# Kernel tuning notes

Measured on AMD Instinct MI355X. Metric: run time of the kernel, lower is better.

The kernel has to match this reference:

```python
import jax, jax.numpy as jnp
import numpy as np


def setup_inputs() -> dict:
    key = jax.random.key(0)
    ks = jax.random.split(key, 6)
    B, L, C = 32, 336, 512
    t = L // 2 + 1  # 169 rfft frequencies; four_l must equal t
    s = 1.0 / np.sqrt(C)
    return {
        "x": jax.random.normal(ks[0], (B, L, C), jnp.float32),
        "Wr": jax.random.normal(ks[1], (t, C, C), jnp.float32) * s,  # real part of complex Linear weights [t, out, in]
        "Wi": jax.random.normal(ks[2], (t, C, C), jnp.float32) * s,  # imag part
        "br": jax.random.normal(ks[3], (t, C), jnp.float32) * s,
        "bi": jax.random.normal(ks[4], (t, C), jnp.float32) * s,
        "weights": jax.random.normal(ks[5], (t,), jnp.float32),
    }


def reference(x, Wr, Wi, br, bi, weights):
    # x: [B, L, C] real. rfft along time with ortho norm -> [B, t, C] complex.
    B, L, C = x.shape
    t = Wr.shape[0]
    n = 2 * (t - 1)  # torch irfft default output length (== L, L even)
    xf = jnp.fft.rfft(x, axis=1, norm='ortho')  # [B, t, C] complex64

    # Per-frequency complex linear: y[b,i,o] = sum_c xf[b,i,c] * W[i,o,c] + b[i,o].
    # This fuses the original repeat + eye-mask + python loop into one batched GEMM.
    W = Wr + 1j * Wi
    b = br + 1j * bi
    y = jnp.einsum('bic,ioc->bio', xf, W) + b[None]  # [B, t, C]

    # The original builds fre[b,i,:,c] as a spectrum that is one-hot at frequency i
    # (value y[b,i,c]) and irffts along the frequency axis (ortho norm). For a one-hot
    # spectrum: irfft(onehot_i * y)[l] = scale_i * Re(y * exp(2*pi*j*i*l/n)) / sqrt(n),
    # with scale_i = 2 except at DC (i=0) and Nyquist (i=t-1) where it is 1
    # (imag parts of DC/Nyquist bins are discarded by C2R, matching torch).
    # Finally ConcatenationWithLearnableCoefficient sums over i with softmax weights,
    # so we fold softmax(weights) * scale_i / sqrt(n) into one coefficient per i.
    i_idx = jnp.arange(t)
    scale = jnp.where((i_idx == 0) | (i_idx == t - 1), 1.0, 2.0).astype(jnp.float32)
    w = jax.nn.softmax(weights)
    coef = w * scale / jnp.sqrt(jnp.float32(n))  # [t]

    l_idx = jnp.arange(n)
    theta = (2.0 * jnp.pi / n) * (i_idx[:, None] * l_idx[None, :]).astype(jnp.float32)  # [t, n]
    cos_m, sin_m = jnp.cos(theta), jnp.sin(theta)

    yr = y.real * coef[None, :, None]
    yi = y.imag * coef[None, :, None]
    # Re(y * e^{j theta}) = yr*cos - yi*sin ; sum over frequencies i -> [B, n, C]
    out = jnp.einsum('bic,il->blc', yr, cos_m) - jnp.einsum('bic,il->blc', yi, sin_m)
    return out
```

## Files before the change

kernel.cpp:

```cpp
#include <hip/hip_runtime.h>
#include <math.h>

typedef short   s16x8  __attribute__((ext_vector_type(8)));
typedef __bf16  bf16x8 __attribute__((ext_vector_type(8)));
typedef float   f32x4  __attribute__((ext_vector_type(4)));

#define T_FREQ 169
#define NN     336
#define CCH    512
#define BB     32
#define TP     176
#define LP     352
#define KP     192

static constexpr size_t OFF_COEF = 0;
static constexpr size_t OFF_FC   = 1024;
static constexpr size_t OFF_FS   = OFF_FC + 124928;
static constexpr size_t OFF_CCOS = OFF_FS + 124928;
static constexpr size_t OFF_CSIN = OFF_CCOS + 130048;
static constexpr size_t OFF_XT   = OFF_CSIN + 130048;
static constexpr size_t OFF_XR   = OFF_XT + (size_t)BB*CCH*LP*2;
static constexpr size_t OFF_XI   = OFF_XR + (size_t)TP*BB*CCH*2;
static constexpr size_t OFF_Y    = OFF_XI + (size_t)TP*BB*CCH*2;

__device__ __forceinline__ unsigned short f2bf(float f){
  unsigned u = __builtin_bit_cast(unsigned, f);
  u = (u + 0x7fffu + ((u >> 16) & 1u)) >> 16;
  return (unsigned short)u;
}

__device__ __forceinline__ f32x4 mfma16(bf16x8 a, bf16x8 b, f32x4 c){
  return __builtin_amdgcn_mfma_f32_16x16x32_bf16(a, b, c, 0, 0, 0);
}

__global__ __launch_bounds__(256) void prep_tables(const float* __restrict__ wts, char* ws){
  float* coef = (float*)(ws + OFF_COEF);
  unsigned short* Fc  = (unsigned short*)(ws + OFF_FC);
  unsigned short* Fs  = (unsigned short*)(ws + OFF_FS);
  unsigned short* Cc  = (unsigned short*)(ws + OFF_CCOS);
  unsigned short* Cs  = (unsigned short*)(ws + OFF_CSIN);
  const float PI2_N = 6.283185307179586f / (float)NN;
  const float inv_sqrt_n = 0.05455447255899809f;

  if (blockIdx.x == 0){
    __shared__ float red[256];
    int tid = threadIdx.x;
    float v = (tid < T_FREQ) ? wts[tid] : -1e30f;
    red[tid] = v; __syncthreads();
    for (int s = 128; s > 0; s >>= 1){ if (tid < s) red[tid] = fmaxf(red[tid], red[tid+s]); __syncthreads(); }
    float mx = red[0]; __syncthreads();
    float e = (tid < T_FREQ) ? expf(v - mx) : 0.f;
    red[tid] = e; __syncthreads();
    for (int s = 128; s > 0; s >>= 1){ if (tid < s) red[tid] += red[tid+s]; __syncthreads(); }
    float ssum = red[0];
    if (tid < T_FREQ){
      float sc = (tid == 0 || tid == T_FREQ-1) ? 1.f : 2.f;
      coef[tid] = (e / ssum) * sc * inv_sqrt_n;
    }
    return;
  }
  int gid = (blockIdx.x - 1) * 256 + threadIdx.x;
  int stride = (gridDim.x - 1) * 256;
  for (int e = gid; e < TP*LP; e += stride){
    int i = e / LP, l = e % LP;
    float c = 0.f, s = 0.f;
    if (l < NN){
      int m = (i * l) % NN;
      float sv, cv; sincosf(PI2_N * (float)m, &sv, &cv);
      c = cv * inv_sqrt_n; s = -sv * inv_sqrt_n;
    }
    Fc[e] = f2bf(c); Fs[e] = f2bf(s);
  }
  for (int e = gid; e < NN*KP; e += stride){
    int l = e / KP, i = e % KP;
    float c = 0.f, s = 0.f;
    if (i < T_FREQ){
      int m = (i * l) % NN;
      float sv, cv; sincosf(PI2_N * (float)m, &sv, &cv);
      c = cv; s = -sv;
    }
    Cc[e] = f2bf(c); Cs[e] = f2bf(s);
  }
}

__global__ __launch_bounds__(256) void transpose_x(const float* __restrict__ x, char* ws){
  unsigned short* xt = (unsigned short*)(ws + OFF_XT);
  __shared__ float tile[32][33];
  int bid = blockIdx.x;
  int b  = bid / (11*16);
  int rm = bid % (11*16);
  int lt = rm / 16, ct = rm % 16;
  int tx = threadIdx.x & 31, ty = threadIdx.x >> 5;
  #pragma unroll
  for (int k = 0; k < 4; ++k){
    int l = lt*32 + ty + k*8;
    int c = ct*32 + tx;
    float v = (l < NN) ? x[((size_t)b*NN + l)*CCH + c] : 0.f;
    tile[ty + k*8][tx] = v;
  }
  __syncthreads();
  #pragma unroll
  for (int k = 0; k < 4; ++k){
    int crow = ct*32 + ty + k*8;
    int lcol = lt*32 + tx;
    xt[((size_t)b*CCH + crow)*LP + lcol] = f2bf(tile[tx][ty + k*8]);
  }
}

__global__ __launch_bounds__(256) void stage_rfft(char* ws){
  const unsigned short* xt = (const unsigned short*)(ws + OFF_XT);
  const unsigned short* Fc = (const unsigned short*)(ws + OFF_FC);
  const unsigned short* Fs = (const unsigned short*)(ws + OFF_FS);
  unsigned short* xr = (unsigned short*)(ws + OFF_XR);
  unsigned short* xi = (unsigned short*)(ws + OFF_XI);

  int b  = blockIdx.x >> 3;
  int c0 = (blockIdx.x & 7) * 64;
  int tid = threadIdx.x, lane = tid & 63, wv = tid >> 6;
  int kg = lane >> 4, ln = lane & 15;
  int c = c0 + wv*16 + ln;

  f32x4 aR[11], aI[11];
  #pragma unroll
  for (int m = 0; m < 11; ++m){ aR[m] = (f32x4){0,0,0,0}; aI[m] = (f32x4){0,0,0,0}; }

  const unsigned short* xrow = xt + ((size_t)b*CCH + c)*LP;
  for (int kk = 0; kk < 11; ++kk){
    int ko = kk*32 + kg*8;
    bf16x8 bx = *(const bf16x8*)(xrow + ko);
    #pragma unroll
    for (int m = 0; m < 11; ++m){
      bf16x8 fc = *(const bf16x8*)(Fc + (size_t)(m*16 + ln)*LP + ko);
      bf16x8 fs = *(const bf16x8*)(Fs + (size_t)(m*16 + ln)*LP + ko);
      aR[m] = mfma16(fc, bx, aR[m]);
      aI[m] = mfma16(fs, bx, aI[m]);
    }
  }
  int rbase = kg*4;
  #pragma unroll
  for (int m = 0; m < 11; ++m){
    #pragma unroll
    for (int r = 0; r < 4; ++r){
      int i = m*16 + rbase + r;
      size_t off = ((size_t)i*BB + b)*CCH + c;
      xr[off] = f2bf(aR[m][r]);
      xi[off] = f2bf(aI[m][r]);
    }
  }
}

__global__ __launch_bounds__(256) void stage_cgemm(const float* __restrict__ Wr, const float* __restrict__ Wi,
                                                   const float* __restrict__ br, const float* __restrict__ bi,
                                                   char* ws){
  const unsigned short* xr = (const unsigned short*)(ws + OFF_XR);
  const unsigned short* xi = (const unsigned short*)(ws + OFF_XI);
  const float* coef = (const float*)(ws + OFF_COEF);
  unsigned int* y = (unsigned int*)(ws + OFF_Y);

  int i  = blockIdx.x >> 2;
  int nb = blockIdx.x & 3;
  int tid = threadIdx.x, lane = tid & 63, wv = tid >> 6;
  int kg = lane >> 4, ln = lane & 15;
  int o0 = nb*128 + wv*32;

  f32x4 accR[2][2], accI[2][2];
  #pragma unroll
  for (int m = 0; m < 2; ++m)
    #pragma unroll
    for (int n = 0; n < 2; ++n){ accR[m][n] = (f32x4){0,0,0,0}; accI[m][n] = (f32x4){0,0,0,0}; }

  const size_t wbase = (size_t)i * CCH * CCH;
  const size_t xbase = (size_t)i * BB * CCH;

  for (int kk = 0; kk < 16; ++kk){
    int ko = kk*32 + kg*8;
    bf16x8 ar[2], ai[2];
    #pragma unroll
    for (int mb = 0; mb < 2; ++mb){
      ar[mb] = *(const bf16x8*)(xr + xbase + (size_t)(mb*16 + ln)*CCH + ko);
      ai[mb] = *(const bf16x8*)(xi + xbase + (size_t)(mb*16 + ln)*CCH + ko);
    }
    #pragma unroll
    for (int nt = 0; nt < 2; ++nt){
      const float* wrp = Wr + wbase + (size_t)(o0 + nt*16 + ln)*CCH + ko;
      const float* wip = Wi + wbase + (size_t)(o0 + nt*16 + ln)*CCH + ko;
      float4 r0 = *(const float4*)(wrp);
      float4 r1 = *(const float4*)(wrp + 4);
      float4 i0 = *(const float4*)(wip);
      float4 i1 = *(const float4*)(wip + 4);
      s16x8 tr, ti;
      tr[0]=f2bf(r0.x); tr[1]=f2bf(r0.y); tr[2]=f2bf(r0.z); tr[3]=f2bf(r0.w);
      tr[4]=f2bf(r1.x); tr[5]=f2bf(r1.y); tr[6]=f2bf(r1.z); tr[7]=f2bf(r1.w);
      ti[0]=f2bf(i0.x); ti[1]=f2bf(i0.y); ti[2]=f2bf(i0.z); ti[3]=f2bf(i0.w);
      ti[4]=f2bf(i1.x); ti[5]=f2bf(i1.y); ti[6]=f2bf(i1.z); ti[7]=f2bf(i1.w);
      s16x8 tin = ti ^ (short)0x8000;
      bf16x8 bwr  = __builtin_bit_cast(bf16x8, tr);
      bf16x8 bwi  = __builtin_bit_cast(bf16x8, ti);
      bf16x8 bwin = __builtin_bit_cast(bf16x8, tin);
      #pragma unroll
      for (int mb = 0; mb < 2; ++mb){
        accR[mb][nt] = mfma16(ar[mb], bwr,  accR[mb][nt]);
        accR[mb][nt] = mfma16(ai[mb], bwin, accR[mb][nt]);
        accI[mb][nt] = mfma16(ar[mb], bwi,  accI[mb][nt]);
        accI[mb][nt] = mfma16(ai[mb], bwr,  accI[mb][nt]);
      }
    }
  }

  float cf = coef[i];
  #pragma unroll
  for (int nt = 0; nt < 2; ++nt){
    int o = o0 + nt*16 + ln;
    float fbr = br[(size_t)i*CCH + o];
    float fbi = bi[(size_t)i*CCH + o];
    #pragma unroll
    for (int mb = 0; mb < 2; ++mb){
      #pragma unroll
      for (int r = 0; r < 4; ++r){
        float vr = (accR[mb][nt][r] + fbr) * cf;
        float vi = (accI[mb][nt][r] + fbi) * cf;
        int bb = mb*16 + kg*4 + r;
        y[((size_t)bb*KP + i)*CCH + o] = (unsigned)f2bf(vr) | ((unsigned)f2bf(vi) << 16);
      }
    }
  }
}

__global__ __launch_bounds__(256) void stage_irfft(const char* ws_c, float* __restrict__ out){
  const char* ws = ws_c;
  const unsigned short* Cc = (const unsigned short*)(ws + OFF_CCOS);
  const unsigned short* Cs = (const unsigned short*)(ws + OFF_CSIN);
  const unsigned int* y = (const unsigned int*)(ws + OFF_Y);

  __shared__ unsigned short lr[64][40];
  __shared__ unsigned short li[64][40];

  int b  = blockIdx.x >> 3;
  int c0 = (blockIdx.x & 7) * 64;
  int tid = threadIdx.x, lane = tid & 63, wv = tid >> 6;
  int kg = lane >> 4, ln = lane & 15;

  f32x4 acc[21];
  #pragma unroll
  for (int m = 0; m < 21; ++m) acc[m] = (f32x4){0,0,0,0};

  for (int kk = 0; kk < 6; ++kk){
    if (kk) __syncthreads();
    #pragma unroll
    for (int q = 0; q < 8; ++q){
      int idx = q*256 + tid;
      int ir = idx >> 6, cc = idx & 63;
      int i = kk*32 + ir;
      unsigned u = (i < T_FREQ) ? y[((size_t)b*KP + i)*CCH + c0 + cc] : 0u;
      lr[cc][ir] = (unsigned short)(u & 0xffffu);
      li[cc][ir] = (unsigned short)(u >> 16);
    }
    __syncthreads();
    int ko = kk*32 + kg*8;
    bf16x8 blr = *(const bf16x8*)(&lr[wv*16 + ln][kg*8]);
    bf16x8 bli = *(const bf16x8*)(&li[wv*16 + ln][kg*8]);
    #pragma unroll
    for (int m = 0; m < 21; ++m){
      bf16x8 ac = *(const bf16x8*)(Cc + (size_t)(m*16 + ln)*KP + ko);
      bf16x8 as = *(const bf16x8*)(Cs + (size_t)(m*16 + ln)*KP + ko);
      acc[m] = mfma16(ac, blr, acc[m]);
      acc[m] = mfma16(as, bli, acc[m]);
    }
  }

  int cdst = c0 + wv*16 + ln;
  #pragma unroll
  for (int m = 0; m < 21; ++m){
    #pragma unroll
    for (int r = 0; r < 4; ++r){
      int l = m*16 + kg*4 + r;
      out[((size_t)b*NN + l)*CCH + cdst] = acc[m][r];
    }
  }
}

extern "C" void kernel_launch(void* const* d_in, const int* in_sizes, int n_in,
                              void* d_out, int out_size, void* d_ws, size_t ws_size,
                              hipStream_t stream){
  const float* x   = (const float*)d_in[0];
  const float* Wr  = (const float*)d_in[1];
  const float* Wi  = (const float*)d_in[2];
  const float* br  = (const float*)d_in[3];
  const float* bi  = (const float*)d_in[4];
  const float* wts = (const float*)d_in[5];
  char* ws = (char*)d_ws;

  prep_tables<<<257, 256, 0, stream>>>(wts, ws);
  transpose_x<<<32*11*16, 256, 0, stream>>>(x, ws);
  stage_rfft<<<256, 256, 0, stream>>>(ws);
  stage_cgemm<<<T_FREQ*4, 256, 0, stream>>>(Wr, Wi, br, bi, ws);
  stage_irfft<<<256, 256, 0, stream>>>(ws, (float*)d_out);
}
```

Baseline: 185.6 us.

## Split FFT stages across more blocks and pipeline weight loads in complex GEMM

The rfft and irfft stages now split their output-row tiles across twice as many blocks, with one overlapping tile computed redundantly, to raise occupancy and cut per-thread accumulator registers. The complex GEMM narrows each wave to 16 output columns, launches twice as many blocks, and double-buffers the fp32 weight loads one k-step ahead so memory latency overlaps MFMA work. Float-to-bf16 conversion now uses the compiler's native cast instead of manual bit rounding. The cost is some duplicated table reads and redundant tile work, plus less reuse of the x operand per block in the GEMM.

```diff
diff --git a/kernel.cpp b/kernel.cpp
--- a/kernel.cpp
+++ b/kernel.cpp
@@ -24,9 +24,14 @@
 static constexpr size_t OFF_Y    = OFF_XI + (size_t)TP*BB*CCH*2;
 
 __device__ __forceinline__ unsigned short f2bf(float f){
-  unsigned u = __builtin_bit_cast(unsigned, f);
-  u = (u + 0x7fffu + ((u >> 16) & 1u)) >> 16;
-  return (unsigned short)u;
+  return __builtin_bit_cast(unsigned short, (__bf16)f);
+}
+
+__device__ __forceinline__ bf16x8 cvt8(float4 lo, float4 hi){
+  bf16x8 r;
+  r[0]=(__bf16)lo.x; r[1]=(__bf16)lo.y; r[2]=(__bf16)lo.z; r[3]=(__bf16)lo.w;
+  r[4]=(__bf16)hi.x; r[5]=(__bf16)hi.y; r[6]=(__bf16)hi.z; r[7]=(__bf16)hi.w;
+  return r;
 }
 
 __device__ __forceinline__ f32x4 mfma16(bf16x8 a, bf16x8 b, f32x4 c){
@@ -114,40 +119,64 @@
   unsigned short* xr = (unsigned short*)(ws + OFF_XR);
   unsigned short* xi = (unsigned short*)(ws + OFF_XI);
 
-  int b  = blockIdx.x >> 3;
-  int c0 = (blockIdx.x & 7) * 64;
+  int bid = blockIdx.x;
+  int b  = bid >> 4;
+  int rm = bid & 15;
+  int c0 = (rm & 7) * 64;
+  int mh = rm >> 3;
+  int mbase = mh * 5;
   int tid = threadIdx.x, lane = tid & 63, wv = tid >> 6;
   int kg = lane >> 4, ln = lane & 15;
   int c = c0 + wv*16 + ln;
 
-  f32x4 aR[11], aI[11];
-  #pragma unroll
-  for (int m = 0; m < 11; ++m){ aR[m] = (f32x4){0,0,0,0}; aI[m] = (f32x4){0,0,0,0}; }
+  f32x4 aR[6], aI[6];
+  #pragma unroll
+  for (int m = 0; m < 6; ++m){ aR[m] = (f32x4){0,0,0,0}; aI[m] = (f32x4){0,0,0,0}; }
 
   const unsigned short* xrow = xt + ((size_t)b*CCH + c)*LP;
   for (int kk = 0; kk < 11; ++kk){
     int ko = kk*32 + kg*8;
     bf16x8 bx = *(const bf16x8*)(xrow + ko);
     #pragma unroll
-    for (int m = 0; m < 11; ++m){
-      bf16x8 fc = *(const bf16x8*)(Fc + (size_t)(m*16 + ln)*LP + ko);
-      bf16x8 fs = *(const bf16x8*)(Fs + (size_t)(m*16 + ln)*LP + ko);
+    for (int m = 0; m < 6; ++m){
+      bf16x8 fc = *(const bf16x8*)(Fc + (size_t)((mbase+m)*16 + ln)*LP + ko);
+      bf16x8 fs = *(const bf16x8*)(Fs + (size_t)((mbase+m)*16 + ln)*LP + ko);
       aR[m] = mfma16(fc, bx, aR[m]);
       aI[m] = mfma16(fs, bx, aI[m]);
     }
   }
   int rbase = kg*4;
   #pragma unroll
-  for (int m = 0; m < 11; ++m){
+  for (int m = 0; m < 6; ++m){
     #pragma unroll
     for (int r = 0; r < 4; ++r){
-      int i = m*16 + rbase + r;
+      int i = (mbase+m)*16 + rbase + r;
       size_t off = ((size_t)i*BB + b)*CCH + c;
       xr[off] = f2bf(aR[m][r]);
       xi[off] = f2bf(aI[m][r]);
     }
   }
 }
+
+#define CGEMM_COMPUTE(W0,W1,V0,V1,KK) do {                                   \
+    int ko_ = (KK)*32 + kb;                                                  \
+    bf16x8 ar0 = *(const bf16x8*)(xrb + (size_t)(ln)*CCH + ko_);             \
+    bf16x8 ar1 = *(const bf16x8*)(xrb + (size_t)(16+ln)*CCH + ko_);          \
+    bf16x8 ai0 = *(const bf16x8*)(xib + (size_t)(ln)*CCH + ko_);             \
+    bf16x8 ai1 = *(const bf16x8*)(xib + (size_t)(16+ln)*CCH + ko_);          \
+    bf16x8 bwr = cvt8(W0,W1);                                                \
+    bf16x8 bwi = cvt8(V0,V1);                                                \
+    bf16x8 bwin = __builtin_bit_cast(bf16x8,                                 \
+        (s16x8)(__builtin_bit_cast(s16x8,bwi) ^ (short)0x8000));             \
+    accR0 = mfma16(ar0, bwr,  accR0);                                        \
+    accR0 = mfma16(ai0, bwin, accR0);                                        \
+    accI0 = mfma16(ar0, bwi,  accI0);                                        \
+    accI0 = mfma16(ai0, bwr,  accI0);                                        \
+    accR1 = mfma16(ar1, bwr,  accR1);                                        \
+    accR1 = mfma16(ai1, bwin, accR1);                                        \
+    accI1 = mfma16(ar1, bwi,  accI1);                                        \
+    accI1 = mfma16(ai1, bwr,  accI1);                                        \
+  } while (0)
 
 __global__ __launch_bounds__(256) void stage_cgemm(const float* __restrict__ Wr, const float* __restrict__ Wi,
                                                    const float* __restrict__ br, const float* __restrict__ bi,
@@ -157,72 +186,56 @@
   const float* coef = (const float*)(ws + OFF_COEF);
   unsigned int* y = (unsigned int*)(ws + OFF_Y);
 
-  int i  = blockIdx.x >> 2;
-  int nb = blockIdx.x & 3;
+  int i  = blockIdx.x >> 3;
+  int nb = blockIdx.x & 7;
   int tid = threadIdx.x, lane = tid & 63, wv = tid >> 6;
   int kg = lane >> 4, ln = lane & 15;
-  int o0 = nb*128 + wv*32;
-
-  f32x4 accR[2][2], accI[2][2];
-  #pragma unroll
-  for (int m = 0; m < 2; ++m)
-    #pragma unroll
-    for (int n = 0; n < 2; ++n){ accR[m][n] = (f32x4){0,0,0,0}; accI[m][n] = (f32x4){0,0,0,0}; }
-
-  const size_t wbase = (size_t)i * CCH * CCH;
-  const size_t xbase = (size_t)i * BB * CCH;
-
-  for (int kk = 0; kk < 16; ++kk){
-    int ko = kk*32 + kg*8;
-    bf16x8 ar[2], ai[2];
-    #pragma unroll
-    for (int mb = 0; mb < 2; ++mb){
-      ar[mb] = *(const bf16x8*)(xr + xbase + (size_t)(mb*16 + ln)*CCH + ko);
-      ai[mb] = *(const bf16x8*)(xi + xbase + (size_t)(mb*16 + ln)*CCH + ko);
-    }
-    #pragma unroll
-    for (int nt = 0; nt < 2; ++nt){
-      const float* wrp = Wr + wbase + (size_t)(o0 + nt*16 + ln)*CCH + ko;
-      const float* wip = Wi + wbase + (size_t)(o0 + nt*16 + ln)*CCH + ko;
-      float4 r0 = *(const float4*)(wrp);
-      float4 r1 = *(const float4*)(wrp + 4);
-      float4 i0 = *(const float4*)(wip);
-      float4 i1 = *(const float4*)(wip + 4);
-      s16x8 tr, ti;
-      tr[0]=f2bf(r0.x); tr[1]=f2bf(r0.y); tr[2]=f2bf(r0.z); tr[3]=f2bf(r0.w);
-      tr[4]=f2bf(r1.x); tr[5]=f2bf(r1.y); tr[6]=f2bf(r1.z); tr[7]=f2bf(r1.w);
-      ti[0]=f2bf(i0.x); ti[1]=f2bf(i0.y); ti[2]=f2bf(i0.z); ti[3]=f2bf(i0.w);
-      ti[4]=f2bf(i1.x); ti[5]=f2bf(i1.y); ti[6]=f2bf(i1.z); ti[7]=f2bf(i1.w);
-      s16x8 tin = ti ^ (short)0x8000;
-      bf16x8 bwr  = __builtin_bit_cast(bf16x8, tr);
-      bf16x8 bwi  = __builtin_bit_cast(bf16x8, ti);
-      bf16x8 bwin = __builtin_bit_cast(bf16x8, tin);
-      #pragma unroll
-      for (int mb = 0; mb < 2; ++mb){
-        accR[mb][nt] = mfma16(ar[mb], bwr,  accR[mb][nt]);
-        accR[mb][nt] = mfma16(ai[mb], bwin, accR[mb][nt]);
-        accI[mb][nt] = mfma16(ar[mb], bwi,  accI[mb][nt]);
-        accI[mb][nt] = mfma16(ai[mb], bwr,  accI[mb][nt]);
-      }
-    }
-  }
-
-  float cf = coef[i];
-  #pragma unroll
-  for (int nt = 0; nt < 2; ++nt){
-    int o = o0 + nt*16 + ln;
-    float fbr = br[(size_t)i*CCH + o];
-    float fbi = bi[(size_t)i*CCH + o];
-    #pragma unroll
-    for (int mb = 0; mb < 2; ++mb){
-      #pragma unroll
-      for (int r = 0; r < 4; ++r){
-        float vr = (accR[mb][nt][r] + fbr) * cf;
-        float vi = (accI[mb][nt][r] + fbi) * cf;
-        int bb = mb*16 + kg*4 + r;
-        y[((size_t)bb*KP + i)*CCH + o] = (unsigned)f2bf(vr) | ((unsigned)f2bf(vi) << 16);
-      }
-    }
+  int o = nb*64 + wv*16 + ln;
+  int kb = kg*8;
+
+  f32x4 accR0 = (f32x4){0,0,0,0}, accR1 = (f32x4){0,0,0,0};
+  f32x4 accI0 = (f32x4){0,0,0,0}, accI1 = (f32x4){0,0,0,0};
+
+  const float* wrk = Wr + (size_t)i*CCH*CCH + (size_t)o*CCH + kb;
+  const float* wik = Wi + (size_t)i*CCH*CCH + (size_t)o*CCH + kb;
+  const unsigned short* xrb = xr + (size_t)i*BB*CCH;
+  const unsigned short* xib = xi + (size_t)i*BB*CCH;
+
+  float4 pa0, pa1, pb0, pb1, qa0, qa1, qb0, qb1;
+  pa0 = *(const float4*)(wrk);     pa1 = *(const float4*)(wrk + 4);
+  pb0 = *(const float4*)(wik);     pb1 = *(const float4*)(wik + 4);
+
+  #pragma unroll
+  for (int kk = 0; kk < 16; kk += 2){
+    {
+      const float* wr1 = wrk + (size_t)(kk+1)*32;
+      const float* wi1 = wik + (size_t)(kk+1)*32;
+      qa0 = *(const float4*)(wr1); qa1 = *(const float4*)(wr1 + 4);
+      qb0 = *(const float4*)(wi1); qb1 = *(const float4*)(wi1 + 4);
+    }
+    CGEMM_COMPUTE(pa0, pa1, pb0, pb1, kk);
+    if (kk + 2 < 16){
+      const float* wr2 = wrk + (size_t)(kk+2)*32;
+      const float* wi2 = wik + (size_t)(kk+2)*32;
+      pa0 = *(const float4*)(wr2); pa1 = *(const float4*)(wr2 + 4);
+      pb0 = *(const float4*)(wi2); pb1 = *(const float4*)(wi2 + 4);
+    }
+    CGEMM_COMPUTE(qa0, qa1, qb0, qb1, kk+1);
+  }
+
+  float cf  = coef[i];
+  float fbr = br[(size_t)i*CCH + o];
+  float fbi = bi[(size_t)i*CCH + o];
+  #pragma unroll
+  for (int r = 0; r < 4; ++r){
+    int bb0 = kg*4 + r;
+    float vr0 = (accR0[r] + fbr) * cf;
+    float vi0 = (accI0[r] + fbi) * cf;
+    y[((size_t)bb0*KP + i)*CCH + o] = (unsigned)f2bf(vr0) | ((unsigned)f2bf(vi0) << 16);
+    int bb1 = 16 + kg*4 + r;
+    float vr1 = (accR1[r] + fbr) * cf;
+    float vi1 = (accI1[r] + fbi) * cf;
+    y[((size_t)bb1*KP + i)*CCH + o] = (unsigned)f2bf(vr1) | ((unsigned)f2bf(vi1) << 16);
   }
 }
 
@@ -235,14 +248,18 @@
   __shared__ unsigned short lr[64][40];
   __shared__ unsigned short li[64][40];
 
-  int b  = blockIdx.x >> 3;
-  int c0 = (blockIdx.x & 7) * 64;
+  int bid = blockIdx.x;
+  int b  = bid >> 4;
+  int rm = bid & 15;
+  int c0 = (rm & 7) * 64;
+  int mh = rm >> 3;
+  int mbase = mh * 10;
   int tid = threadIdx.x, lane = tid & 63, wv = tid >> 6;
   int kg = lane >> 4, ln = lane & 15;
 
-  f32x4 acc[21];
-  #pragma unroll
-  for (int m = 0; m < 21; ++m) acc[m] = (f32x4){0,0,0,0};
+  f32x4 acc[11];
+  #pragma unroll
+  for (int m = 0; m < 11; ++m) acc[m] = (f32x4){0,0,0,0};
 
   for (int kk = 0; kk < 6; ++kk){
     if (kk) __syncthreads();
@@ -260,9 +277,9 @@
     bf16x8 blr = *(const bf16x8*)(&lr[wv*16 + ln][kg*8]);
     bf16x8 bli = *(const bf16x8*)(&li[wv*16 + ln][kg*8]);
     #pragma unroll
-    for (int m = 0; m < 21; ++m){
-      bf16x8 ac = *(const bf16x8*)(Cc + (size_t)(m*16 + ln)*KP + ko);
-      bf16x8 as = *(const bf16x8*)(Cs + (size_t)(m*16 + ln)*KP + ko);
+    for (int m = 0; m < 11; ++m){
+      bf16x8 ac = *(const bf16x8*)(Cc + (size_t)((mbase+m)*16 + ln)*KP + ko);
+      bf16x8 as = *(const bf16x8*)(Cs + (size_t)((mbase+m)*16 + ln)*KP + ko);
       acc[m] = mfma16(ac, blr, acc[m]);
       acc[m] = mfma16(as, bli, acc[m]);
     }
@@ -270,10 +287,10 @@
 
   int cdst = c0 + wv*16 + ln;
   #pragma unroll
-  for (int m = 0; m < 21; ++m){
+  for (int m = 0; m < 11; ++m){
     #pragma unroll
     for (int r = 0; r < 4; ++r){
-      int l = m*16 + kg*4 + r;
+      int l = (mbase+m)*16 + kg*4 + r;
       out[((size_t)b*NN + l)*CCH + cdst] = acc[m][r];
     }
   }
@@ -292,7 +309,7 @@
 
   prep_tables<<<257, 256, 0, stream>>>(wts, ws);
   transpose_x<<<32*11*16, 256, 0, stream>>>(x, ws);
-  stage_rfft<<<256, 256, 0, stream>>>(ws);
-  stage_cgemm<<<T_FREQ*4, 256, 0, stream>>>(Wr, Wi, br, bi, ws);
-  stage_irfft<<<256, 256, 0, stream>>>(ws, (float*)d_out);
-}
+  stage_rfft<<<512, 256, 0, stream>>>(ws);
+  stage_cgemm<<<T_FREQ*8, 256, 0, stream>>>(Wr, Wi, br, bi, ws);
+  stage_irfft<<<512, 256, 0, stream>>>(ws, (float*)d_out);
+}
```

Result: slower. 190.8 us (+2.8%).
